# Kernel optimization log

Measured on AMD Instinct MI355X. Metric: run time of the kernel, lower is better.

## Reference

```python
import jax, jax.numpy as jnp
import numpy as np

NUM_GROUPS = 32
EPS = 1e-6


def group_norm(x, scale, bias):
    # x: (b, c, t, h, w)
    b, c, t, h, w = x.shape
    xg = x.reshape(b, NUM_GROUPS, c // NUM_GROUPS, t, h, w)
    mean = jnp.mean(xg, axis=(2, 3, 4, 5), keepdims=True)
    var = jnp.var(xg, axis=(2, 3, 4, 5), keepdims=True)
    xg = (xg - mean) * jax.lax.rsqrt(var + EPS)
    xn = xg.reshape(b, c, t, h, w)
    return xn * scale[None, :, None, None, None] + bias[None, :, None, None, None]


def conv1x1(x, w, bvec):
    # 1x1x1 Conv3d == per-position linear over channels
    return jnp.einsum('oc,bcthw->bothw', w, x) + bvec[None, :, None, None, None]


def setup_inputs() -> dict:
    key = jax.random.key(0)
    ks = jax.random.split(key, 11)
    b, c, t, h, w = 2, 256, 4, 32, 32
    x = jax.random.normal(ks[0], (b, c, t, h, w), dtype=jnp.float32)
    s = 1.0 / np.sqrt(c)
    return {
        'x': x,
        'gn_scale': jnp.ones((c,), jnp.float32),
        'gn_bias': jnp.zeros((c,), jnp.float32),
        'wq': jax.random.normal(ks[1], (c, c), jnp.float32) * s,
        'bq': jax.random.normal(ks[2], (c,), jnp.float32) * 0.01,
        'wk': jax.random.normal(ks[3], (c, c), jnp.float32) * s,
        'bk': jax.random.normal(ks[4], (c,), jnp.float32) * 0.01,
        'wv': jax.random.normal(ks[5], (c, c), jnp.float32) * s,
        'bv': jax.random.normal(ks[6], (c,), jnp.float32) * 0.01,
        'wp': jax.random.normal(ks[7], (c, c), jnp.float32) * s,
        'bp': jax.random.normal(ks[8], (c,), jnp.float32) * 0.01,
    }


def reference(x, gn_scale, gn_bias, wq, bq, wk, bk, wv, bv, wp, bp):
    b, c, t, h, w = x.shape
    n = t * h * w
    h_ = group_norm(x, gn_scale, gn_bias)
    q = conv1x1(h_, wq, bq).reshape(b, c, n)  # (b, c, n)
    k = conv1x1(h_, wk, bk).reshape(b, c, n)
    v = conv1x1(h_, wv, bv).reshape(b, c, n)
    scale = jnp.asarray(int(c) ** (-0.5), x.dtype)
    # attn[b, i, j] = sum_c q[b,c,i] k[b,c,j]
    attn = jnp.einsum('bci,bcj->bij', q, k) * scale
    attn = jax.nn.softmax(attn, axis=2)
    # A[b, c, i] = sum_j v[b,c,j] attn[b,i,j]
    A = jnp.einsum('bcj,bij->bci', v, attn).reshape(b, c, t, h, w)
    A = conv1x1(A, wp, bp)
    return x + A
```

## Files before the change

kernel.cpp:

```cpp
#include <hip/hip_runtime.h>
#include <hip/hip_bf16.h>
#include <math.h>

#define BB 2
#define CC 256
#define GG 32
#define NN 4096
#define EPSF 1e-6f
#define JSPLIT 8
#define JBLK (NN / JSPLIT)
#define CH 32
#define NT (JBLK / CH)
#define QTILE 128
#define LOG2E 1.4426950408889634f

typedef _Float16 f16x8 __attribute__((ext_vector_type(8)));
typedef float f32x4 __attribute__((ext_vector_type(4)));

static __device__ __forceinline__ unsigned short f2h_bits(float f) {
    _Float16 h = (_Float16)f;
    return __builtin_bit_cast(unsigned short, h);
}
static __device__ __forceinline__ unsigned pkh2(float a, float b) {
    return __builtin_bit_cast(unsigned, __builtin_amdgcn_cvt_pkrtz(a, b));
}
static __device__ __forceinline__ void gload16(const void* g, void* l) {
    __builtin_amdgcn_global_load_lds(
        (const __attribute__((address_space(1))) void*)g,
        (__attribute__((address_space(3))) void*)l, 16, 0, 0);
}

__global__ __launch_bounds__(256) void prep_w16_kernel(
    const float* __restrict__ wq, const float* __restrict__ wk,
    const float* __restrict__ wv, const float* __restrict__ wp,
    unsigned short* __restrict__ w16)
{
    int m = blockIdx.y;
    const float* src = (m == 0) ? wq : (m == 1) ? wk : (m == 2) ? wv : wp;
    float scale = (m == 0) ? 0.0625f * LOG2E : 1.0f;
    int idx = blockIdx.x * 256 + threadIdx.x;
    float4 v = ((const float4*)src)[idx];
    union { _Float16 h[4]; uint2 u; } pk;
    pk.h[0] = (_Float16)(v.x * scale);
    pk.h[1] = (_Float16)(v.y * scale);
    pk.h[2] = (_Float16)(v.z * scale);
    pk.h[3] = (_Float16)(v.w * scale);
    *(uint2*)(w16 + (size_t)m * CC * CC + (size_t)idx * 4) = pk.u;
}

__global__ __launch_bounds__(256) void gn_part_kernel(
    const float* __restrict__ x, float2* __restrict__ part)
{
    int g = blockIdx.x, p = blockIdx.y, b = blockIdx.z;
    const float* base = x + ((size_t)b * CC + (size_t)g * 8) * NN + (size_t)p * 8192;
    int t = threadIdx.x;
    float s = 0.f, ss = 0.f;
    for (int idx = t; idx < 2048; idx += 256) {
        float4 v4 = ((const float4*)base)[idx];
        s  += v4.x + v4.y + v4.z + v4.w;
        ss += v4.x*v4.x + v4.y*v4.y + v4.z*v4.z + v4.w*v4.w;
    }
    for (int off = 32; off; off >>= 1) {
        s  += __shfl_down(s,  off);
        ss += __shfl_down(ss, off);
    }
    __shared__ float red[8];
    int wid = t >> 6;
    if ((t & 63) == 0) { red[wid*2] = s; red[wid*2+1] = ss; }
    __syncthreads();
    if (t == 0) {
        part[(b*GG + g)*4 + p] = make_float2(red[0]+red[2]+red[4]+red[6],
                                             red[1]+red[3]+red[5]+red[7]);
    }
}

__global__ __launch_bounds__(256) void proj_qkv_kernel(
    const float* __restrict__ x, const float* __restrict__ sc,
    const float* __restrict__ bi, const float2* __restrict__ part,
    const unsigned short* __restrict__ w16,
    const float* __restrict__ bq, const float* __restrict__ bk,
    const float* __restrict__ bv,
    unsigned short* __restrict__ qT, unsigned short* __restrict__ kT,
    unsigned short* __restrict__ vC)
{
    int b  = blockIdx.y;
    int i0 = blockIdx.x * 32;
    int t  = threadIdx.x;
    __shared__ unsigned short htile[32 * 256];
    __shared__ float s_mean[GG], s_rstd[GG], s_sc[CC], s_bi[CC];
    if (t < GG) {
        float2 p0 = part[(b*GG + t)*4 + 0];
        float2 p1 = part[(b*GG + t)*4 + 1];
        float2 p2 = part[(b*GG + t)*4 + 2];
        float2 p3 = part[(b*GG + t)*4 + 3];
        float S  = p0.x + p1.x + p2.x + p3.x;
        float SS = p0.y + p1.y + p2.y + p3.y;
        float mean = S / 32768.f;
        float var  = SS / 32768.f - mean * mean;
        s_mean[t] = mean;
        s_rstd[t] = rsqrtf(var + EPSF);
    }
    s_sc[t] = sc[t];
    s_bi[t] = bi[t];
    __syncthreads();

    char* hw = (char*)htile;
    int nq = (t & 7) * 4;
    int cq = (t >> 3) * 4;
    #pragma unroll
    for (int k = 0; k < 2; k++) {
        int c0 = cq + k * 128;
        float4 xr[4];
        float aa[4], dd[4];
        #pragma unroll
        for (int e = 0; e < 4; e++) {
            int c = c0 + e;
            xr[e] = *(const float4*)(x + ((size_t)b*CC + c)*NN + i0 + nq);
            aa[e] = s_rstd[c >> 3] * s_sc[c];
            dd[e] = s_bi[c] - s_mean[c >> 3] * aa[e];
        }
        #pragma unroll
        for (int j = 0; j < 4; j++) {
            int row = nq + j;
            union { _Float16 h[4]; uint2 u; } pk;
            pk.h[0] = (_Float16)(((const float*)&xr[0])[j] * aa[0] + dd[0]);
            pk.h[1] = (_Float16)(((const float*)&xr[1])[j] * aa[1] + dd[1]);
            pk.h[2] = (_Float16)(((const float*)&xr[2])[j] * aa[2] + dd[2]);
            pk.h[3] = (_Float16)(((const float*)&xr[3])[j] * aa[3] + dd[3]);
            int off = row*512 + (((c0 >> 3) ^ (row & 7)) << 4) + (c0 & 7) * 2;
            *(uint2*)(hw + off) = pk.u;
        }
    }
    __syncthreads();

    int lane = t & 63, w = t >> 6;
    int col = lane & 15, grp = lane >> 4;
    const char* hr = (const char*)htile;

    #pragma unroll
    for (int p = 0; p < 2; p++) {
        const unsigned short* wgt = w16 + (size_t)p * CC * CC;
        const float* bias = p ? bk : bq;
        unsigned short* outp = (p ? kT : qT) + (size_t)b * NN * CC;
        float osc = p ? 1.0f : 0.0625f * LOG2E;
        #pragma unroll
        for (int ot = 0; ot < 4; ot++) {
            int ow = ot * 64 + w * 16;
            f32x4 acc[2];
            acc[0] = (f32x4){0.f,0.f,0.f,0.f};
            acc[1] = (f32x4){0.f,0.f,0.f,0.f};
            #pragma unroll
            for (int ck = 0; ck < 8; ck++) {
                f16x8 af = *(const f16x8*)(wgt + (size_t)(ow + col)*CC + ck*32 + grp*8);
                #pragma unroll
                for (int it = 0; it < 2; it++) {
                    int row = it*16 + col;
                    f16x8 bf = *(const f16x8*)(hr + row*512 + (((ck*4 + grp) ^ (row & 7)) << 4));
                    acc[it] = __builtin_amdgcn_mfma_f32_16x16x32_f16(af, bf, acc[it], 0, 0, 0);
                }
            }
            int obase = ow + grp * 4;
            float b0 = bias[obase]*osc, b1 = bias[obase+1]*osc,
                  b2 = bias[obase+2]*osc, b3 = bias[obase+3]*osc;
            #pragma unroll
            for (int it = 0; it < 2; it++) {
                int i = i0 + it*16 + col;
                union { _Float16 h[4]; uint2 u; } pk;
                pk.h[0] = (_Float16)(acc[it][0] + b0);
                pk.h[1] = (_Float16)(acc[it][1] + b1);
                pk.h[2] = (_Float16)(acc[it][2] + b2);
                pk.h[3] = (_Float16)(acc[it][3] + b3);
                *(uint2*)(outp + (size_t)i*CC + obase) = pk.u;
            }
        }
    }
    {
        const unsigned short* wgt = w16 + (size_t)2 * CC * CC;
        unsigned short* outp = vC + (size_t)b * CC * NN;
        int ibase = (w & 1) * 16;
        #pragma unroll
        for (int gg = 0; gg < 2; gg++) {
            int og = (w >> 1) * 2 + gg;
            f32x4 acc[4];
            #pragma unroll
            for (int ot = 0; ot < 4; ot++) acc[ot] = (f32x4){0.f,0.f,0.f,0.f};
            #pragma unroll
            for (int ck = 0; ck < 8; ck++) {
                int row = ibase + col;
                f16x8 af = *(const f16x8*)(hr + row*512 + (((ck*4 + grp) ^ (row & 7)) << 4));
                #pragma unroll
                for (int ot = 0; ot < 4; ot++) {
                    f16x8 bf = *(const f16x8*)(wgt + (size_t)(og*64 + ot*16 + col)*CC + ck*32 + grp*8);
                    acc[ot] = __builtin_amdgcn_mfma_f32_16x16x32_f16(af, bf, acc[ot], 0, 0, 0);
                }
            }
            int iw = i0 + ibase + grp * 4;
            #pragma unroll
            for (int ot = 0; ot < 4; ot++) {
                int o = og*64 + ot*16 + col;
                float bo = bv[o];
                union { _Float16 h[4]; uint2 u; } pk;
                pk.h[0] = (_Float16)(acc[ot][0] + bo);
                pk.h[1] = (_Float16)(acc[ot][1] + bo);
                pk.h[2] = (_Float16)(acc[ot][2] + bo);
                pk.h[3] = (_Float16)(acc[ot][3] + bo);
                *(uint2*)(outp + (size_t)o*NN + iw) = pk.u;
            }
        }
    }
}

#define WAITV(n) asm volatile("s_waitcnt vmcnt(" #n ")" ::: "memory")
#define SBAR() do { __builtin_amdgcn_sched_barrier(0); __builtin_amdgcn_s_barrier(); \
                    __builtin_amdgcn_sched_barrier(0); } while (0)
#define STAGE_K(tt, bb) do { int _j = jlo + (tt)*CH; _Pragma("unroll") \
    for (int e = 0; e < 4; e++) gload16(kb + (size_t)_j*CC + koff[e], &bufK[bb][(4*w + e)*512]); } while (0)
#define STAGE_V(tt, bb) do { int _j = jlo + (tt)*CH; _Pragma("unroll") \
    for (int e = 0; e < 4; e++) gload16(vb + voff[e] + _j, &bufV[bb][(4*w + e)*512]); } while (0)

__global__ __launch_bounds__(256, 2) void attn_kernel(
    const unsigned short* __restrict__ qT,
    const unsigned short* __restrict__ kT,
    const unsigned short* __restrict__ vC,
    unsigned short* __restrict__ pO,
    float2* __restrict__ ml)
{
    int qt = blockIdx.x, s = blockIdx.y, b = blockIdx.z;
    int tid = threadIdx.x, w = tid >> 6, lane = tid & 63;
    int l15 = lane & 15, grp = lane >> 4;
    int q0 = qt * QTILE + w * 32;
    int jlo = s * JBLK;

    __shared__ unsigned short bufK[2][8192];
    __shared__ unsigned short bufV[2][8192];

    const unsigned short* qb = qT + (size_t)b * NN * CC;
    const unsigned short* kb = kT + (size_t)b * NN * CC;
    const unsigned short* vb = vC + (size_t)b * CC * NN;

    f16x8 qfA[8], qfB[8];
    #pragma unroll
    for (int ck = 0; ck < 8; ck++) {
        qfA[ck] = *(const f16x8*)(qb + (size_t)(q0 + l15)*CC + ck*32 + grp*8);
        qfB[ck] = *(const f16x8*)(qb + (size_t)(q0 + 16 + l15)*CC + ck*32 + grp*8);
    }

    int koff[4], voff[4];
    #pragma unroll
    for (int e = 0; e < 4; e++) {
        int blk = (4*w + e)*64 + lane;
        int kj = blk >> 5, kcb = blk & 31;
        koff[e] = kj*CC + ((kcb ^ (kj & 7)) * 8);
        int vc = blk >> 2, vcb = blk & 3;
        voff[e] = vc*NN + ((vcb ^ ((vc >> 1) & 3)) * 8);
    }
    int kru = l15 * 512;
    int krw = (l15 & 7) << 4;
    int g16 = grp << 4;
    int vrb = l15*64 + ((grp ^ ((l15 >> 1) & 3)) << 4);

    f32x4 OA[16], OB[16];
    #pragma unroll
    for (int ck = 0; ck < 16; ck++) {
        OA[ck] = (f32x4){0.f,0.f,0.f,0.f};
        OB[ck] = (f32x4){0.f,0.f,0.f,0.f};
    }
    float mA = -1e30f, lA = 0.f, mB = -1e30f, lB = 0.f;

    STAGE_K(0, 0);
    STAGE_V(0, 0);
    STAGE_K(1, 1);

    for (int t = 0; t < NT; t++) {
        int cur = t & 1;
        if (t < NT - 1) WAITV(8); else WAITV(4);
        SBAR();
        if (t + 1 < NT) STAGE_V(t + 1, cur ^ 1);

        const char* kbase = (const char*)&bufK[cur][0];
        const char* vbase = (const char*)&bufV[cur][0];

        f32x4 sA0 = (f32x4){0.f,0.f,0.f,0.f}, sA1 = (f32x4){0.f,0.f,0.f,0.f};
        f32x4 sB0 = (f32x4){0.f,0.f,0.f,0.f}, sB1 = (f32x4){0.f,0.f,0.f,0.f};
        __builtin_amdgcn_s_setprio(1);
        #pragma unroll
        for (int ck = 0; ck < 8; ck++) {
            int cx = ((ck*64) | g16) ^ krw;
            f16x8 k0 = *(const f16x8*)(kbase + kru + cx);
            f16x8 k1 = *(const f16x8*)(kbase + 8192 + kru + cx);
            sA0 = __builtin_amdgcn_mfma_f32_16x16x32_f16(k0, qfA[ck], sA0, 0, 0, 0);
            sA1 = __builtin_amdgcn_mfma_f32_16x16x32_f16(k1, qfA[ck], sA1, 0, 0, 0);
            sB0 = __builtin_amdgcn_mfma_f32_16x16x32_f16(k0, qfB[ck], sB0, 0, 0, 0);
            sB1 = __builtin_amdgcn_mfma_f32_16x16x32_f16(k1, qfB[ck], sB1, 0, 0, 0);
        }
        __builtin_amdgcn_s_setprio(0);

        f16x8 pfA, pfB;
        {
            float x0 = fmaxf(fmaxf(sA0[0], sA0[1]), fmaxf(sA0[2], sA0[3]));
            float x1 = fmaxf(fmaxf(sA1[0], sA1[1]), fmaxf(sA1[2], sA1[3]));
            float mx = fmaxf(x0, x1);
            mx = fmaxf(mx, __shfl_xor(mx, 16));
            mx = fmaxf(mx, __shfl_xor(mx, 32));
            bool up = !__all(mx <= mA);
            if (up) {
                float mn = fmaxf(mA, mx);
                float f = exp2f(mA - mn);
                mA = mn;
                lA *= f;
                int fb = (lane & 48) | (grp << 2);
                float fs0 = __shfl(f, fb),   fs1 = __shfl(f, fb+1);
                float fs2 = __shfl(f, fb+2), fs3 = __shfl(f, fb+3);
                f32x4 fv = (f32x4){fs0, fs1, fs2, fs3};
                #pragma unroll
                for (int ck = 0; ck < 16; ck++) OA[ck] *= fv;
            }
            sA0[0] = exp2f(sA0[0] - mA); sA0[1] = exp2f(sA0[1] - mA);
            sA0[2] = exp2f(sA0[2] - mA); sA0[3] = exp2f(sA0[3] - mA);
            sA1[0] = exp2f(sA1[0] - mA); sA1[1] = exp2f(sA1[1] - mA);
            sA1[2] = exp2f(sA1[2] - mA); sA1[3] = exp2f(sA1[3] - mA);
            float ps = ((sA0[0]+sA0[1]) + (sA0[2]+sA0[3])) + ((sA1[0]+sA1[1]) + (sA1[2]+sA1[3]));
            ps += __shfl_xor(ps, 16);
            ps += __shfl_xor(ps, 32);
            lA += ps;
            unsigned pk0 = pkh2(sA0[0], sA0[1]);
            unsigned pk1 = pkh2(sA0[2], sA0[3]);
            unsigned pk2 = pkh2(sA1[0], sA1[1]);
            unsigned pk3 = pkh2(sA1[2], sA1[3]);
            int srcA = (((grp << 1)    ) & 3) * 16 + l15;
            int srcB = (((grp << 1) + 1) & 3) * 16 + l15;
            bool lo = (grp < 2);
            unsigned u0A = __shfl(pk0, srcA), u2A = __shfl(pk2, srcA);
            unsigned u1A = __shfl(pk1, srcA), u3A = __shfl(pk3, srcA);
            unsigned u0B = __shfl(pk0, srcB), u2B = __shfl(pk2, srcB);
            unsigned u1B = __shfl(pk1, srcB), u3B = __shfl(pk3, srcB);
            uint4 pu;
            pu.x = lo ? u0A : u2A;
            pu.y = lo ? u1A : u3A;
            pu.z = lo ? u0B : u2B;
            pu.w = lo ? u1B : u3B;
            pfA = __builtin_bit_cast(f16x8, pu);
        }
        {
            float x0 = fmaxf(fmaxf(sB0[0], sB0[1]), fmaxf(sB0[2], sB0[3]));
            float x1 = fmaxf(fmaxf(sB1[0], sB1[1]), fmaxf(sB1[2], sB1[3]));
            float mx = fmaxf(x0, x1);
            mx = fmaxf(mx, __shfl_xor(mx, 16));
            mx = fmaxf(mx, __shfl_xor(mx, 32));
            bool up = !__all(mx <= mB);
            if (up) {
                float mn = fmaxf(mB, mx);
                float f = exp2f(mB - mn);
                mB = mn;
                lB *= f;
                int fb = (lane & 48) | (grp << 2);
                float fs0 = __shfl(f, fb),   fs1 = __shfl(f, fb+1);
                float fs2 = __shfl(f, fb+2), fs3 = __shfl(f, fb+3);
                f32x4 fv = (f32x4){fs0, fs1, fs2, fs3};
                #pragma unroll
                for (int ck = 0; ck < 16; ck++) OB[ck] *= fv;
            }
            sB0[0] = exp2f(sB0[0] - mB); sB0[1] = exp2f(sB0[1] - mB);
            sB0[2] = exp2f(sB0[2] - mB); sB0[3] = exp2f(sB0[3] - mB);
            sB1[0] = exp2f(sB1[0] - mB); sB1[1] = exp2f(sB1[1] - mB);
            sB1[2] = exp2f(sB1[2] - mB); sB1[3] = exp2f(sB1[3] - mB);
            float ps = ((sB0[0]+sB0[1]) + (sB0[2]+sB0[3])) + ((sB1[0]+sB1[1]) + (sB1[2]+sB1[3]));
            ps += __shfl_xor(ps, 16);
            ps += __shfl_xor(ps, 32);
            lB += ps;
            unsigned pk0 = pkh2(sB0[0], sB0[1]);
            unsigned pk1 = pkh2(sB0[2], sB0[3]);
            unsigned pk2 = pkh2(sB1[0], sB1[1]);
            unsigned pk3 = pkh2(sB1[2], sB1[3]);
            int srcA = (((grp << 1)    ) & 3) * 16 + l15;
            int srcB = (((grp << 1) + 1) & 3) * 16 + l15;
            bool lo = (grp < 2);
            unsigned u0A = __shfl(pk0, srcA), u2A = __shfl(pk2, srcA);
            unsigned u1A = __shfl(pk1, srcA), u3A = __shfl(pk3, srcA);
            unsigned u0B = __shfl(pk0, srcB), u2B = __shfl(pk2, srcB);
            unsigned u1B = __shfl(pk1, srcB), u3B = __shfl(pk3, srcB);
            uint4 pu;
            pu.x = lo ? u0A : u2A;
            pu.y = lo ? u1A : u3A;
            pu.z = lo ? u0B : u2B;
            pu.w = lo ? u1B : u3B;
            pfB = __builtin_bit_cast(f16x8, pu);
        }

        if (t < NT - 1) WAITV(8); else WAITV(0);
        SBAR();
        if (t + 2 < NT) STAGE_K(t + 2, cur);

        __builtin_amdgcn_s_setprio(1);
        #pragma unroll
        for (int ck = 0; ck < 16; ck++) {
            f16x8 vf = *(const f16x8*)(vbase + ck*1024 + vrb);
            OA[ck] = __builtin_amdgcn_mfma_f32_16x16x32_f16(pfA, vf, OA[ck], 0, 0, 0);
            OB[ck] = __builtin_amdgcn_mfma_f32_16x16x32_f16(pfB, vf, OB[ck], 0, 0, 0);
        }
        __builtin_amdgcn_s_setprio(0);
    }

    float invA = 1.f / lA, invB = 1.f / lB;
    int ib = (lane & 48) | (grp << 2);
    float a0 = __shfl(invA, ib),   a1 = __shfl(invA, ib+1);
    float a2 = __shfl(invA, ib+2), a3 = __shfl(invA, ib+3);
    float b0 = __shfl(invB, ib),   b1 = __shfl(invB, ib+1);
    float b2 = __shfl(invB, ib+2), b3 = __shfl(invB, ib+3);
    unsigned short* po = pO + ((size_t)(s*BB + b)*NN + q0) * CC;
    #pragma unroll
    for (int ck = 0; ck < 16; ck++) {
        po[(size_t)(grp*4+0)*CC + ck*16 + l15] = f2h_bits(OA[ck][0] * a0);
        po[(size_t)(grp*4+1)*CC + ck*16 + l15] = f2h_bits(OA[ck][1] * a1);
        po[(size_t)(grp*4+2)*CC + ck*16 + l15] = f2h_bits(OA[ck][2] * a2);
        po[(size_t)(grp*4+3)*CC + ck*16 + l15] = f2h_bits(OA[ck][3] * a3);
        po[(size_t)(16 + grp*4+0)*CC + ck*16 + l15] = f2h_bits(OB[ck][0] * b0);
        po[(size_t)(16 + grp*4+1)*CC + ck*16 + l15] = f2h_bits(OB[ck][1] * b1);
        po[(size_t)(16 + grp*4+2)*CC + ck*16 + l15] = f2h_bits(OB[ck][2] * b2);
        po[(size_t)(16 + grp*4+3)*CC + ck*16 + l15] = f2h_bits(OB[ck][3] * b3);
    }
    if (lane < 16)
        ml[(size_t)(s*BB + b)*NN + q0 + lane] = make_float2(mA, lA);
    else if (lane < 32)
        ml[(size_t)(s*BB + b)*NN + q0 + 16 + l15] = make_float2(mB, lB);
}

__global__ __launch_bounds__(256) void attn_merge_kernel(
    const unsigned short* __restrict__ pO, const float2* __restrict__ ml,
    unsigned short* __restrict__ aT)
{
    int t = threadIdx.x;
    int qrow = blockIdx.x * 16 + (t >> 4);
    int c0 = (t & 15) * 16;
    float M = -1e30f;
    float m8[JSPLIT], l8[JSPLIT];
    #pragma unroll
    for (int s = 0; s < JSPLIT; s++) {
        float2 v = ml[(size_t)s*BB*NN + qrow];
        m8[s] = v.x; l8[s] = v.y;
        M = fmaxf(M, v.x);
    }
    float W = 0.f, wt[JSPLIT];
    #pragma unroll
    for (int s = 0; s < JSPLIT; s++) { wt[s] = l8[s] * exp2f(m8[s] - M); W += wt[s]; }
    float iW = 1.f / W;
    float acc[16];
    #pragma unroll
    for (int e = 0; e < 16; e++) acc[e] = 0.f;
    #pragma unroll
    for (int s = 0; s < JSPLIT; s++) {
        const unsigned short* p = pO + ((size_t)s*BB*NN + qrow)*CC + c0;
        f16x8 a0 = *(const f16x8*)p;
        f16x8 a1 = *(const f16x8*)(p + 8);
        float ws = wt[s] * iW;
        #pragma unroll
        for (int e = 0; e < 8; e++) {
            acc[e]     += ws * (float)a0[e];
            acc[e + 8] += ws * (float)a1[e];
        }
    }
    union { _Float16 h[8]; uint4 u; } o0, o1;
    #pragma unroll
    for (int e = 0; e < 8; e++) { o0.h[e] = (_Float16)acc[e]; o1.h[e] = (_Float16)acc[e+8]; }
    unsigned short* dst = aT + (size_t)qrow*CC + c0;
    *(uint4*)dst = o0.u;
    *(uint4*)(dst + 8) = o1.u;
}

__global__ __launch_bounds__(256) void proj_out_kernel(
    const unsigned short* __restrict__ aT,
    const unsigned short* __restrict__ wp16, const float* __restrict__ bp,
    const float* __restrict__ x, float* __restrict__ out)
{
    int b = blockIdx.z;
    int i0 = blockIdx.x * 64, o0 = blockIdx.y * 64;
    int lane = threadIdx.x & 63, wid = threadIdx.x >> 6;
    int col = lane & 15, grp = lane >> 4;
    int ibase = i0 + wid * 16;
    const unsigned short* ab = aT + (size_t)b*NN*CC;
    f32x4 acc[4];
    for (int ot = 0; ot < 4; ot++) acc[ot] = (f32x4){0.f,0.f,0.f,0.f};
    for (int ck = 0; ck < 8; ck++) {
        f16x8 af = *(const f16x8*)(ab + (size_t)(ibase + col)*CC + ck*32 + grp*8);
        for (int ot = 0; ot < 4; ot++) {
            f16x8 bf = *(const f16x8*)(wp16 + (size_t)(o0 + ot*16 + col)*CC + ck*32 + grp*8);
            acc[ot] = __builtin_amdgcn_mfma_f32_16x16x32_f16(af, bf, acc[ot], 0, 0, 0);
        }
    }
    int iw = ibase + grp * 4;
    for (int ot = 0; ot < 4; ot++) {
        int o = o0 + ot*16 + col;
        float bo = bp[o];
        size_t base = (size_t)b*CC*NN + (size_t)o*NN + iw;
        float4 x4 = *(const float4*)(x + base);
        float4 r;
        r.x = x4.x + acc[ot][0] + bo;
        r.y = x4.y + acc[ot][1] + bo;
        r.z = x4.z + acc[ot][2] + bo;
        r.w = x4.w + acc[ot][3] + bo;
        *(float4*)(out + base) = r;
    }
}

extern "C" void kernel_launch(void* const* d_in, const int* in_sizes, int n_in,
                              void* d_out, int out_size, void* d_ws, size_t ws_size,
                              hipStream_t stream) {
    const float* x  = (const float*)d_in[0];
    const float* gs = (const float*)d_in[1];
    const float* gb = (const float*)d_in[2];
    const float* wq = (const float*)d_in[3];
    const float* bq = (const float*)d_in[4];
    const float* wk = (const float*)d_in[5];
    const float* bk = (const float*)d_in[6];
    const float* wv = (const float*)d_in[7];
    const float* bv = (const float*)d_in[8];
    const float* wp = (const float*)d_in[9];
    const float* bp = (const float*)d_in[10];
    float* out = (float*)d_out;

    char* ws = (char*)d_ws;
    const size_t sz = (size_t)BB * NN * CC * sizeof(unsigned short);
    unsigned short* qT  = (unsigned short*)(ws + sz);
    unsigned short* kT  = (unsigned short*)(ws + 2*sz);
    unsigned short* vC  = (unsigned short*)(ws + 3*sz);
    unsigned short* aT  = (unsigned short*)(ws + 4*sz);
    unsigned short* w16 = (unsigned short*)(ws + 5*sz);
    float2* part        = (float2*)(ws + 5*sz + 512*1024);
    float2* ml          = (float2*)(ws + 5*sz + 768*1024);
    unsigned short* pO  = (unsigned short*)(ws + 5*sz + 1280*1024);

    prep_w16_kernel<<<dim3(CC*CC/4/256, 4), 256, 0, stream>>>(wq, wk, wv, wp, w16);
    gn_part_kernel<<<dim3(GG, 4, BB), 256, 0, stream>>>(x, part);
    proj_qkv_kernel<<<dim3(NN/32, BB), 256, 0, stream>>>(x, gs, gb, part, w16,
                                                         bq, bk, bv, qT, kT, vC);
    attn_kernel<<<dim3(NN/QTILE, JSPLIT, BB), 256, 0, stream>>>(qT, kT, vC, pO, ml);
    attn_merge_kernel<<<dim3(BB*NN/16), 256, 0, stream>>>(pO, ml, aT);
    proj_out_kernel<<<dim3(NN/64, CC/64, BB), 256, 0, stream>>>(aT, w16 + 3*CC*CC, bp, x, out);
}
```

Baseline: 141.1 us.

## Restructure attention kernel around 32x32 MFMA scores with LDS P transpose

Computes QK^T scores with 32x32x16 MFMAs into a 16-wide accumulator per wave, replacing four 16x16x32 MFMA chains and their duplicated two-half softmax. The probability tile now goes through per-wave LDS instead of lane shuffles. The PV product swaps operand roles and stores packed halves. The online softmax only rescales when the running max grows by more than 8. The hand-tuned vmcnt-counted K/V pipeline is replaced by simple double buffering with a __syncthreads per tile, which may expose load latency.

```diff
diff --git a/kernel.cpp b/kernel.cpp
--- a/kernel.cpp
+++ b/kernel.cpp
@@ -16,6 +16,7 @@
 
 typedef _Float16 f16x8 __attribute__((ext_vector_type(8)));
 typedef float f32x4 __attribute__((ext_vector_type(4)));
+typedef float f32x16 __attribute__((ext_vector_type(16)));
 
 static __device__ __forceinline__ unsigned short f2h_bits(float f) {
     _Float16 h = (_Float16)f;
@@ -210,9 +211,6 @@
     }
 }
 
-#define WAITV(n) asm volatile("s_waitcnt vmcnt(" #n ")" ::: "memory")
-#define SBAR() do { __builtin_amdgcn_sched_barrier(0); __builtin_amdgcn_s_barrier(); \
-                    __builtin_amdgcn_sched_barrier(0); } while (0)
 #define STAGE_K(tt, bb) do { int _j = jlo + (tt)*CH; _Pragma("unroll") \
     for (int e = 0; e < 4; e++) gload16(kb + (size_t)_j*CC + koff[e], &bufK[bb][(4*w + e)*512]); } while (0)
 #define STAGE_V(tt, bb) do { int _j = jlo + (tt)*CH; _Pragma("unroll") \
@@ -227,23 +225,23 @@
 {
     int qt = blockIdx.x, s = blockIdx.y, b = blockIdx.z;
     int tid = threadIdx.x, w = tid >> 6, lane = tid & 63;
-    int l15 = lane & 15, grp = lane >> 4;
+    int l31 = lane & 31, hi = lane >> 5;
+    int col = lane & 15, grp = lane >> 4;
     int q0 = qt * QTILE + w * 32;
     int jlo = s * JBLK;
 
-    __shared__ unsigned short bufK[2][8192];
-    __shared__ unsigned short bufV[2][8192];
+    __shared__ __align__(16) unsigned short bufK[2][8192];
+    __shared__ __align__(16) unsigned short bufV[2][8192];
+    __shared__ __align__(16) unsigned short plds[4 * 1280];
 
     const unsigned short* qb = qT + (size_t)b * NN * CC;
     const unsigned short* kb = kT + (size_t)b * NN * CC;
     const unsigned short* vb = vC + (size_t)b * CC * NN;
 
-    f16x8 qfA[8], qfB[8];
-    #pragma unroll
-    for (int ck = 0; ck < 8; ck++) {
-        qfA[ck] = *(const f16x8*)(qb + (size_t)(q0 + l15)*CC + ck*32 + grp*8);
-        qfB[ck] = *(const f16x8*)(qb + (size_t)(q0 + 16 + l15)*CC + ck*32 + grp*8);
-    }
+    f16x8 qf[16];
+    #pragma unroll
+    for (int ck = 0; ck < 16; ck++)
+        qf[ck] = *(const f16x8*)(qb + (size_t)(q0 + l31)*CC + ck*16 + hi*8);
 
     int koff[4], voff[4];
     #pragma unroll
@@ -254,175 +252,105 @@
         int vc = blk >> 2, vcb = blk & 3;
         voff[e] = vc*NN + ((vcb ^ ((vc >> 1) & 3)) * 8);
     }
-    int kru = l15 * 512;
-    int krw = (l15 & 7) << 4;
-    int g16 = grp << 4;
-    int vrb = l15*64 + ((grp ^ ((l15 >> 1) & 3)) << 4);
-
-    f32x4 OA[16], OB[16];
-    #pragma unroll
-    for (int ck = 0; ck < 16; ck++) {
-        OA[ck] = (f32x4){0.f,0.f,0.f,0.f};
-        OB[ck] = (f32x4){0.f,0.f,0.f,0.f};
-    }
-    float mA = -1e30f, lA = 0.f, mB = -1e30f, lB = 0.f;
+    int kru = l31 * 512;
+    int kx  = l31 & 7;
+    int vrb = col*64 + ((grp ^ ((col >> 1) & 3)) << 4);
+    char* pw  = (char*)plds + w*2560 + l31*80 + 8*hi;
+    const char* prd = (const char*)plds + w*2560;
+
+    f32x4 O0[16], O1[16];
+    #pragma unroll
+    for (int ct = 0; ct < 16; ct++) {
+        O0[ct] = (f32x4){0.f,0.f,0.f,0.f};
+        O1[ct] = (f32x4){0.f,0.f,0.f,0.f};
+    }
+    float m = -1e30f, l = 0.f;
 
     STAGE_K(0, 0);
     STAGE_V(0, 0);
-    STAGE_K(1, 1);
+    __syncthreads();
 
     for (int t = 0; t < NT; t++) {
         int cur = t & 1;
-        if (t < NT - 1) WAITV(8); else WAITV(4);
-        SBAR();
-        if (t + 1 < NT) STAGE_V(t + 1, cur ^ 1);
-
+        if (t + 1 < NT) {
+            STAGE_K(t + 1, cur ^ 1);
+            STAGE_V(t + 1, cur ^ 1);
+        }
         const char* kbase = (const char*)&bufK[cur][0];
         const char* vbase = (const char*)&bufV[cur][0];
 
-        f32x4 sA0 = (f32x4){0.f,0.f,0.f,0.f}, sA1 = (f32x4){0.f,0.f,0.f,0.f};
-        f32x4 sB0 = (f32x4){0.f,0.f,0.f,0.f}, sB1 = (f32x4){0.f,0.f,0.f,0.f};
+        f32x16 S;
+        #pragma unroll
+        for (int r = 0; r < 16; r++) S[r] = 0.f;
         __builtin_amdgcn_s_setprio(1);
         #pragma unroll
-        for (int ck = 0; ck < 8; ck++) {
-            int cx = ((ck*64) | g16) ^ krw;
-            f16x8 k0 = *(const f16x8*)(kbase + kru + cx);
-            f16x8 k1 = *(const f16x8*)(kbase + 8192 + kru + cx);
-            sA0 = __builtin_amdgcn_mfma_f32_16x16x32_f16(k0, qfA[ck], sA0, 0, 0, 0);
-            sA1 = __builtin_amdgcn_mfma_f32_16x16x32_f16(k1, qfA[ck], sA1, 0, 0, 0);
-            sB0 = __builtin_amdgcn_mfma_f32_16x16x32_f16(k0, qfB[ck], sB0, 0, 0, 0);
-            sB1 = __builtin_amdgcn_mfma_f32_16x16x32_f16(k1, qfB[ck], sB1, 0, 0, 0);
+        for (int ck = 0; ck < 16; ck++) {
+            f16x8 kf = *(const f16x8*)(kbase + kru + ((((ck*2) | hi) ^ kx) << 4));
+            S = __builtin_amdgcn_mfma_f32_32x32x16_f16(kf, qf[ck], S, 0, 0, 0);
         }
         __builtin_amdgcn_s_setprio(0);
 
-        f16x8 pfA, pfB;
+        float x0 = fmaxf(fmaxf(S[0], S[1]), fmaxf(S[2], S[3]));
+        float x1 = fmaxf(fmaxf(S[4], S[5]), fmaxf(S[6], S[7]));
+        float x2 = fmaxf(fmaxf(S[8], S[9]), fmaxf(S[10], S[11]));
+        float x3 = fmaxf(fmaxf(S[12], S[13]), fmaxf(S[14], S[15]));
+        float mh = fmaxf(fmaxf(x0, x1), fmaxf(x2, x3));
+        float mx = fmaxf(mh, __shfl_xor(mh, 32));
+
+        if (!__all(mx <= m + 8.f)) {
+            float mn = fmaxf(m, mx);
+            float f = exp2f(m - mn);
+            m = mn;
+            l *= f;
+            float fq0 = __shfl(f, col);
+            float fq1 = __shfl(f, 16 + col);
+            #pragma unroll
+            for (int ct = 0; ct < 16; ct++) { O0[ct] *= fq0; O1[ct] *= fq1; }
+        }
+
+        #pragma unroll
+        for (int r = 0; r < 16; r++) S[r] = exp2f(S[r] - m);
+        float ps = (((S[0]+S[1]) + (S[2]+S[3])) + ((S[4]+S[5]) + (S[6]+S[7])))
+                 + (((S[8]+S[9]) + (S[10]+S[11])) + ((S[12]+S[13]) + (S[14]+S[15])));
+        l += ps + __shfl_xor(ps, 32);
+
         {
-            float x0 = fmaxf(fmaxf(sA0[0], sA0[1]), fmaxf(sA0[2], sA0[3]));
-            float x1 = fmaxf(fmaxf(sA1[0], sA1[1]), fmaxf(sA1[2], sA1[3]));
-            float mx = fmaxf(x0, x1);
-            mx = fmaxf(mx, __shfl_xor(mx, 16));
-            mx = fmaxf(mx, __shfl_xor(mx, 32));
-            bool up = !__all(mx <= mA);
-            if (up) {
-                float mn = fmaxf(mA, mx);
-                float f = exp2f(mA - mn);
-                mA = mn;
-                lA *= f;
-                int fb = (lane & 48) | (grp << 2);
-                float fs0 = __shfl(f, fb),   fs1 = __shfl(f, fb+1);
-                float fs2 = __shfl(f, fb+2), fs3 = __shfl(f, fb+3);
-                f32x4 fv = (f32x4){fs0, fs1, fs2, fs3};
-                #pragma unroll
-                for (int ck = 0; ck < 16; ck++) OA[ck] *= fv;
-            }
-            sA0[0] = exp2f(sA0[0] - mA); sA0[1] = exp2f(sA0[1] - mA);
-            sA0[2] = exp2f(sA0[2] - mA); sA0[3] = exp2f(sA0[3] - mA);
-            sA1[0] = exp2f(sA1[0] - mA); sA1[1] = exp2f(sA1[1] - mA);
-            sA1[2] = exp2f(sA1[2] - mA); sA1[3] = exp2f(sA1[3] - mA);
-            float ps = ((sA0[0]+sA0[1]) + (sA0[2]+sA0[3])) + ((sA1[0]+sA1[1]) + (sA1[2]+sA1[3]));
-            ps += __shfl_xor(ps, 16);
-            ps += __shfl_xor(ps, 32);
-            lA += ps;
-            unsigned pk0 = pkh2(sA0[0], sA0[1]);
-            unsigned pk1 = pkh2(sA0[2], sA0[3]);
-            unsigned pk2 = pkh2(sA1[0], sA1[1]);
-            unsigned pk3 = pkh2(sA1[2], sA1[3]);
-            int srcA = (((grp << 1)    ) & 3) * 16 + l15;
-            int srcB = (((grp << 1) + 1) & 3) * 16 + l15;
-            bool lo = (grp < 2);
-            unsigned u0A = __shfl(pk0, srcA), u2A = __shfl(pk2, srcA);
-            unsigned u1A = __shfl(pk1, srcA), u3A = __shfl(pk3, srcA);
-            unsigned u0B = __shfl(pk0, srcB), u2B = __shfl(pk2, srcB);
-            unsigned u1B = __shfl(pk1, srcB), u3B = __shfl(pk3, srcB);
-            uint4 pu;
-            pu.x = lo ? u0A : u2A;
-            pu.y = lo ? u1A : u3A;
-            pu.z = lo ? u0B : u2B;
-            pu.w = lo ? u1B : u3B;
-            pfA = __builtin_bit_cast(f16x8, pu);
-        }
-        {
-            float x0 = fmaxf(fmaxf(sB0[0], sB0[1]), fmaxf(sB0[2], sB0[3]));
-            float x1 = fmaxf(fmaxf(sB1[0], sB1[1]), fmaxf(sB1[2], sB1[3]));
-            float mx = fmaxf(x0, x1);
-            mx = fmaxf(mx, __shfl_xor(mx, 16));
-            mx = fmaxf(mx, __shfl_xor(mx, 32));
-            bool up = !__all(mx <= mB);
-            if (up) {
-                float mn = fmaxf(mB, mx);
-                float f = exp2f(mB - mn);
-                mB = mn;
-                lB *= f;
-                int fb = (lane & 48) | (grp << 2);
-                float fs0 = __shfl(f, fb),   fs1 = __shfl(f, fb+1);
-                float fs2 = __shfl(f, fb+2), fs3 = __shfl(f, fb+3);
-                f32x4 fv = (f32x4){fs0, fs1, fs2, fs3};
-                #pragma unroll
-                for (int ck = 0; ck < 16; ck++) OB[ck] *= fv;
-            }
-            sB0[0] = exp2f(sB0[0] - mB); sB0[1] = exp2f(sB0[1] - mB);
-            sB0[2] = exp2f(sB0[2] - mB); sB0[3] = exp2f(sB0[3] - mB);
-            sB1[0] = exp2f(sB1[0] - mB); sB1[1] = exp2f(sB1[1] - mB);
-            sB1[2] = exp2f(sB1[2] - mB); sB1[3] = exp2f(sB1[3] - mB);
-            float ps = ((sB0[0]+sB0[1]) + (sB0[2]+sB0[3])) + ((sB1[0]+sB1[1]) + (sB1[2]+sB1[3]));
-            ps += __shfl_xor(ps, 16);
-            ps += __shfl_xor(ps, 32);
-            lB += ps;
-            unsigned pk0 = pkh2(sB0[0], sB0[1]);
-            unsigned pk1 = pkh2(sB0[2], sB0[3]);
-            unsigned pk2 = pkh2(sB1[0], sB1[1]);
-            unsigned pk3 = pkh2(sB1[2], sB1[3]);
-            int srcA = (((grp << 1)    ) & 3) * 16 + l15;
-            int srcB = (((grp << 1) + 1) & 3) * 16 + l15;
-            bool lo = (grp < 2);
-            unsigned u0A = __shfl(pk0, srcA), u2A = __shfl(pk2, srcA);
-            unsigned u1A = __shfl(pk1, srcA), u3A = __shfl(pk3, srcA);
-            unsigned u0B = __shfl(pk0, srcB), u2B = __shfl(pk2, srcB);
-            unsigned u1B = __shfl(pk1, srcB), u3B = __shfl(pk3, srcB);
-            uint4 pu;
-            pu.x = lo ? u0A : u2A;
-            pu.y = lo ? u1A : u3A;
-            pu.z = lo ? u0B : u2B;
-            pu.w = lo ? u1B : u3B;
-            pfB = __builtin_bit_cast(f16x8, pu);
-        }
-
-        if (t < NT - 1) WAITV(8); else WAITV(0);
-        SBAR();
-        if (t + 2 < NT) STAGE_K(t + 2, cur);
-
+            unsigned* pr = (unsigned*)pw;
+            pr[0]  = pkh2(S[0],  S[1]);   pr[1]  = pkh2(S[2],  S[3]);
+            pr[4]  = pkh2(S[4],  S[5]);   pr[5]  = pkh2(S[6],  S[7]);
+            pr[8]  = pkh2(S[8],  S[9]);   pr[9]  = pkh2(S[10], S[11]);
+            pr[12] = pkh2(S[12], S[13]);  pr[13] = pkh2(S[14], S[15]);
+        }
+        asm volatile("s_waitcnt lgkmcnt(0)" ::: "memory");
+        __builtin_amdgcn_sched_barrier(0);
+
+        f16x8 y0 = *(const f16x8*)(prd + col*80 + grp*16);
+        f16x8 y1 = *(const f16x8*)(prd + (16 + col)*80 + grp*16);
         __builtin_amdgcn_s_setprio(1);
         #pragma unroll
-        for (int ck = 0; ck < 16; ck++) {
-            f16x8 vf = *(const f16x8*)(vbase + ck*1024 + vrb);
-            OA[ck] = __builtin_amdgcn_mfma_f32_16x16x32_f16(pfA, vf, OA[ck], 0, 0, 0);
-            OB[ck] = __builtin_amdgcn_mfma_f32_16x16x32_f16(pfB, vf, OB[ck], 0, 0, 0);
+        for (int ct = 0; ct < 16; ct++) {
+            f16x8 xf = *(const f16x8*)(vbase + ct*1024 + vrb);
+            O0[ct] = __builtin_amdgcn_mfma_f32_16x16x32_f16(xf, y0, O0[ct], 0, 0, 0);
+            O1[ct] = __builtin_amdgcn_mfma_f32_16x16x32_f16(xf, y1, O1[ct], 0, 0, 0);
         }
         __builtin_amdgcn_s_setprio(0);
-    }
-
-    float invA = 1.f / lA, invB = 1.f / lB;
-    int ib = (lane & 48) | (grp << 2);
-    float a0 = __shfl(invA, ib),   a1 = __shfl(invA, ib+1);
-    float a2 = __shfl(invA, ib+2), a3 = __shfl(invA, ib+3);
-    float b0 = __shfl(invB, ib),   b1 = __shfl(invB, ib+1);
-    float b2 = __shfl(invB, ib+2), b3 = __shfl(invB, ib+3);
+        __syncthreads();
+    }
+
+    float inv = 1.f / l;
+    float iq0 = __shfl(inv, col);
+    float iq1 = __shfl(inv, 16 + col);
     unsigned short* po = pO + ((size_t)(s*BB + b)*NN + q0) * CC;
     #pragma unroll
-    for (int ck = 0; ck < 16; ck++) {
-        po[(size_t)(grp*4+0)*CC + ck*16 + l15] = f2h_bits(OA[ck][0] * a0);
-        po[(size_t)(grp*4+1)*CC + ck*16 + l15] = f2h_bits(OA[ck][1] * a1);
-        po[(size_t)(grp*4+2)*CC + ck*16 + l15] = f2h_bits(OA[ck][2] * a2);
-        po[(size_t)(grp*4+3)*CC + ck*16 + l15] = f2h_bits(OA[ck][3] * a3);
-        po[(size_t)(16 + grp*4+0)*CC + ck*16 + l15] = f2h_bits(OB[ck][0] * b0);
-        po[(size_t)(16 + grp*4+1)*CC + ck*16 + l15] = f2h_bits(OB[ck][1] * b1);
-        po[(size_t)(16 + grp*4+2)*CC + ck*16 + l15] = f2h_bits(OB[ck][2] * b2);
-        po[(size_t)(16 + grp*4+3)*CC + ck*16 + l15] = f2h_bits(OB[ck][3] * b3);
-    }
-    if (lane < 16)
-        ml[(size_t)(s*BB + b)*NN + q0 + lane] = make_float2(mA, lA);
-    else if (lane < 32)
-        ml[(size_t)(s*BB + b)*NN + q0 + 16 + l15] = make_float2(mB, lB);
+    for (int ct = 0; ct < 16; ct++) {
+        int c = ct*16 + grp*4;
+        *(unsigned*)(po + (size_t)col*CC + c)            = pkh2(O0[ct][0]*iq0, O0[ct][1]*iq0);
+        *(unsigned*)(po + (size_t)col*CC + c + 2)        = pkh2(O0[ct][2]*iq0, O0[ct][3]*iq0);
+        *(unsigned*)(po + (size_t)(16 + col)*CC + c)     = pkh2(O1[ct][0]*iq1, O1[ct][1]*iq1);
+        *(unsigned*)(po + (size_t)(16 + col)*CC + c + 2) = pkh2(O1[ct][2]*iq1, O1[ct][3]*iq1);
+    }
+    if (lane < 32)
+        ml[(size_t)(s*BB + b)*NN + q0 + lane] = make_float2(m, l);
 }
 
 __global__ __launch_bounds__(256) void attn_merge_kernel(
```

Result: faster. 125.0 us (-11.4%).
